# Kernel optimization log

Hardware: AMD Instinct MI355X
Metric: run time of the kernel (lower is better)

The kernel has to match this reference:

```python
import jax, jax.numpy as jnp
import numpy as np

N, D_FEAT, P, E, L, H, D = 20000, 256, 3, 60000, 4, 8, 32  # d = H*D = 256


def _l2norm(x, axis):
    return x / jnp.maximum(jnp.linalg.norm(x, axis=axis, keepdims=True), 1e-12)


def _gru_last_hidden(edata, w_ih, w_hh, b_ih, b_hh):
    # edata: [E, L, d]; torch nn.GRU gate math, return final hidden [E, d]
    d = w_hh.shape[1]
    def step(h, x):
        gi = x @ w_ih.T + b_ih          # [E, 3d]
        gh = h @ w_hh.T + b_hh
        i_r, i_z, i_n = jnp.split(gi, 3, axis=-1)
        h_r, h_z, h_n = jnp.split(gh, 3, axis=-1)
        r = jax.nn.sigmoid(i_r + h_r)
        z = jax.nn.sigmoid(i_z + h_z)
        n = jnp.tanh(i_n + r * h_n)
        return (1.0 - z) * n + z * h, None
    h0 = jnp.zeros((edata.shape[0], d), edata.dtype)
    h, _ = jax.lax.scan(step, h0, jnp.swapaxes(edata, 0, 1))
    return h


def setup_inputs() -> dict:
    key = jax.random.key(0)
    ks = jax.random.split(key, 10)
    d = H * D
    s = 1.0 / np.sqrt(d)
    return {
        "features": jax.random.normal(ks[0], (N, D_FEAT), jnp.float32),
        "gru_w_ih": jax.random.uniform(ks[1], (P, 3 * d, d), jnp.float32, -s, s),
        "gru_w_hh": jax.random.uniform(ks[2], (P, 3 * d, d), jnp.float32, -s, s),
        "gru_b_ih": jax.random.uniform(ks[3], (P, 3 * d), jnp.float32, -s, s),
        "gru_b_hh": jax.random.uniform(ks[4], (P, 3 * d), jnp.float32, -s, s),
        "fc1_w": jax.random.normal(ks[5], (D, D), jnp.float32) * (1.414 / np.sqrt(D)),
        "fc2": jax.random.normal(ks[6], (H, D), jnp.float32) * (1.414 / np.sqrt(D)),
        "edge_metapath_indices": jax.random.randint(ks[7], (P, E, L), 0, N),
        "edge_dst": jax.random.randint(ks[8], (P, E), 0, N),
    }


def reference(features, gru_w_ih, gru_w_hh, gru_b_ih, gru_b_hh, fc1_w, fc2,
              edge_metapath_indices, edge_dst):
    # node features, normalized across heads (F.normalize default dim=1)
    ft = _l2norm(features.reshape(N, H, D), axis=1)          # [N, H, D]
    metapath_outs = []
    for p in range(P):  # small fixed loop over structurally distinct metapaths
        edata = features[edge_metapath_indices[p]]           # [E, L, d] gather
        hidden = _gru_last_hidden(edata, gru_w_ih[p], gru_w_hh[p],
                                  gru_b_ih[p], gru_b_hh[p])  # [E, d]
        eft = _l2norm(hidden.reshape(E, H, D), axis=1)       # [E, H, D]
        dst = edge_dst[p]                                    # [E]
        sim = jnp.sum(eft * ft[dst], axis=-1)                # [E, H]
        a = jax.nn.softmax(sim, axis=-1)[..., None]          # softmax over heads (faithful)
        nft = jax.ops.segment_sum(eft * a, dst, num_segments=N)  # [N, H, D]
        metapath_outs.append(nft)
    h = jnp.stack(metapath_outs, axis=0)                     # [P, N, H, D]
    # semantic attention across metapaths: fc1 (no bias) then fc2 scoring
    s = jnp.mean(jnp.sum(jnp.tanh(jnp.einsum('pnhd,ed->pnhe', h, fc1_w)) * fc2,
                         axis=(2, 3)), axis=1)               # [P]
    beta = jax.nn.softmax(s)
    out = jnp.einsum('p,pnhd->nhd', beta, h).reshape(N, H * D)
    return out
```

## Files before the change

### kernel.cpp

```cpp
#include <hip/hip_runtime.h>
#include <math.h>


typedef unsigned short u16;
typedef unsigned int u32;
typedef __bf16 bf16x8 __attribute__((ext_vector_type(8)));
typedef short short8 __attribute__((ext_vector_type(8)));
typedef float f32x4 __attribute__((ext_vector_type(4)));

#define N_NODES 20000
#define P_META 3
#define E_EDGES 60000
#define L_STEPS 4
#define DMODEL 256
#define G3 768
#define M_TILE 32
#define TILES_PER_P 1875
#define G_TILES 313

__device__ __forceinline__ float bf2f(u16 b) {
  u32 u = ((u32)b) << 16; float f; __builtin_memcpy(&f, &u, 4); return f;
}
__device__ __forceinline__ u16 f2bf(float f) {
  u32 u; __builtin_memcpy(&u, &f, 4);
  return (u16)((u + 0x7FFFu + ((u >> 16) & 1u)) >> 16);
}
__device__ __forceinline__ u16 f2h(float f) {
  _Float16 h = (_Float16)f; u16 u; __builtin_memcpy(&u, &h, 2); return u;
}
__device__ __forceinline__ float h2f(u16 u) {
  _Float16 h; __builtin_memcpy(&h, &u, 2); return (float)h;
}
__device__ __forceinline__ short8 load8(const void* base, int isbf, size_t off) {
  if (isbf) return *(const short8*)((const u16*)base + off);
  const float* f = (const float*)base + off;
  const float4 a = *(const float4*)f;
  const float4 b = *(const float4*)(f + 4);
  short8 r;
  r[0] = (short)f2bf(a.x); r[1] = (short)f2bf(a.y);
  r[2] = (short)f2bf(a.z); r[3] = (short)f2bf(a.w);
  r[4] = (short)f2bf(b.x); r[5] = (short)f2bf(b.y);
  r[6] = (short)f2bf(b.z); r[7] = (short)f2bf(b.w);
  return r;
}
__device__ __forceinline__ float loadS(const void* base, int isbf, size_t off) {
  return isbf ? bf2f(((const u16*)base)[off]) : ((const float*)base)[off];
}
static __device__ __forceinline__ f32x4 mfma16(short8 a, short8 b, f32x4 c) {
  return __builtin_amdgcn_mfma_f32_16x16x32_bf16(
      __builtin_bit_cast(bf16x8, a), __builtin_bit_cast(bf16x8, b), c, 0, 0, 0);
}
__device__ __forceinline__ float sigm(float x) { return 1.0f / (1.0f + __expf(-x)); }
__device__ __forceinline__ float ftanh(float x) { return 1.0f - 2.0f / (__expf(2.0f * x) + 1.0f); }

__global__ void sniff_kernel(const void* __restrict__ feat, int* __restrict__ flag) {
  const int i = threadIdx.x;
  const u16 e = ((const u16*)feat)[2 * i];
  const int ex = (e >> 7) & 0xFF;
  const bool sane = (e == 0) || (ex >= 103 && ex <= 143);
  const unsigned long long b = __ballot(sane);
  if (i == 0) *flag = (__popcll(b) >= 32) ? 1 : 0;
}

__global__ void pack_weights_kernel(const void* __restrict__ w_ih,
                                    const void* __restrict__ w_hh,
                                    u16* __restrict__ Wpk,
                                    const int* __restrict__ dflag) {
  const int isbf = *dflag;
  const int g = blockIdx.x * 256 + threadIdx.x;
  const int fb = g >> 6, ln = g & 63;
  const int k0 = fb & 7, c = (fb >> 3) & 15, pm = fb >> 7;
  const int p = pm / 6, mat = pm - p * 6;
  const int gate = (mat >= 3) ? mat - 3 : mat;
  const void* W = (mat >= 3) ? w_hh : w_ih;
  const size_t src = ((size_t)p * G3 + gate * 256 + c * 16 + (ln & 15)) * DMODEL
                     + k0 * 32 + (ln >> 4) * 8;
  short8 v = load8(W, isbf, src);
  *(short8*)(Wpk + (size_t)fb * 512 + ln * 8) = v;
}

__global__ void pack_feat_kernel(const void* __restrict__ features,
                                 u16* __restrict__ Fpk,
                                 float* __restrict__ invf,
                                 const int* __restrict__ dflag) {
  const int isbf = *dflag;
  const int n = blockIdx.x * 8 + (threadIdx.x >> 5);
  const int dd = threadIdx.x & 31;
  float v[8]; float ss = 0.f;
  #pragma unroll
  for (int hh = 0; hh < 8; ++hh) {
    v[hh] = loadS(features, isbf, (size_t)n * DMODEL + hh * 32 + dd);
    ss += v[hh] * v[hh];
  }
  invf[(size_t)n * 32 + dd] = 1.0f / fmaxf(sqrtf(ss), 1e-12f);
  #pragma unroll
  for (int hh = 0; hh < 8; ++hh)
    Fpk[(size_t)n * DMODEL + hh * 32 + dd] = f2bf(v[hh]);
}

__global__ void pack_bias_kernel(const void* __restrict__ b_ih,
                                 const void* __restrict__ b_hh,
                                 float* __restrict__ bpk,
                                 const int* __restrict__ dflag) {
  const int isbf = *dflag;
  const int g = blockIdx.x * 256 + threadIdx.x;
  const int p = g / 1536, r = g - p * 1536;
  const int gi = r >> 8, j = r & 255;
  const float v = (gi < 3) ? loadS(b_ih, isbf, (size_t)p * G3 + gi * 256 + j)
                           : loadS(b_hh, isbf, (size_t)p * G3 + (gi - 3) * 256 + j);
  bpk[g] = v;
}

__global__ __launch_bounds__(256, 4) void gih_kernel(
    const u16* __restrict__ Fpk, const u16* __restrict__ Wpk,
    const float* __restrict__ bpk, u16* __restrict__ Gpk,
    u16* __restrict__ H1pk, int p0, int multi)
{
  __shared__ u16 Xb[64 * 256];
  __shared__ float Bs[1536];
  const int tid = threadIdx.x;
  const int bx = blockIdx.x;
  int pb = 0, tile = bx;
  if (multi) { pb = bx / G_TILES; tile = bx - pb * G_TILES; }
  const int p = p0 + pb;
  u16* Gp  = Gpk  + (size_t)pb * (size_t)N_NODES * 1024;
  u16* H1p = H1pk + (size_t)pb * (size_t)N_NODES * DMODEL;
  const int r0 = tile * 64;
  const int wv = tid >> 6, ln = tid & 63;
  const int n16 = ln & 15, quad = ln >> 4;
  const int cbase = wv * 4;

  for (int i = tid; i < 1536; i += 256) Bs[i] = bpk[(size_t)p * 1536 + i];

  const int m4 = tid >> 2, seg = tid & 3, swm = m4 & 7;
  {
    int rr = r0 + m4; if (rr >= N_NODES) rr = N_NODES - 1;
    const u16* frp = Fpk + (size_t)rr * DMODEL;
    #pragma unroll
    for (int u = 0; u < 8; ++u) {
      short8 xv = *(const short8*)(frp + (seg * 8 + u) * 8);
      *(short8*)(Xb + m4 * 256 + (((seg * 8 + u) ^ swm) << 3)) = xv;
    }
  }
  __syncthreads();

  #pragma unroll 1
  for (int ci = 0; ci < 4; ++ci) {
    const int c = cbase + ci;
    const f32x4 z4 = {0.f, 0.f, 0.f, 0.f};
    f32x4 aR[4], aZ[4], aN[4];
    #pragma unroll
    for (int rt = 0; rt < 4; ++rt) { aR[rt] = z4; aZ[rt] = z4; aN[rt] = z4; }
    const u16* wb0 = Wpk + ((size_t)(p * 6 * 16 + c) * 8) * 512 + ln * 8;
    #pragma unroll 2
    for (int k0 = 0; k0 < 8; ++k0) {
      const int un = (((k0 * 4 + quad) ^ (n16 & 7)) << 3);
      const u16* xr = Xb + n16 * 256 + un;
      short8 x0 = *(const short8*)(xr);
      short8 x1 = *(const short8*)(xr + 4096);
      short8 x2 = *(const short8*)(xr + 8192);
      short8 x3 = *(const short8*)(xr + 12288);
      const u16* wk = wb0 + k0 * 512;
      short8 b0 = *(const short8*)(wk);
      short8 b1 = *(const short8*)(wk + 65536);
      short8 b2 = *(const short8*)(wk + 131072);
      aR[0] = mfma16(x0, b0, aR[0]); aR[1] = mfma16(x1, b0, aR[1]);
      aR[2] = mfma16(x2, b0, aR[2]); aR[3] = mfma16(x3, b0, aR[3]);
      aZ[0] = mfma16(x0, b1, aZ[0]); aZ[1] = mfma16(x1, b1, aZ[1]);
      aZ[2] = mfma16(x2, b1, aZ[2]); aZ[3] = mfma16(x3, b1, aZ[3]);
      aN[0] = mfma16(x0, b2, aN[0]); aN[1] = mfma16(x1, b2, aN[1]);
      aN[2] = mfma16(x2, b2, aN[2]); aN[3] = mfma16(x3, b2, aN[3]);
    }
    const int j = c * 16 + n16;
    const float br  = Bs[j],        bz  = Bs[256 + j],  bn  = Bs[512 + j];
    const float bhr = Bs[768 + j],  bhz = Bs[1024 + j], bhn = Bs[1280 + j];
    #pragma unroll
    for (int rt = 0; rt < 4; ++rt) {
      #pragma unroll
      for (int i = 0; i < 4; ++i) {
        const int row = r0 + rt * 16 + quad * 4 + i;
        if (row < N_NODES) {
          const float grb = aR[rt][i] + br + bhr;
          const float gzb = aZ[rt][i] + bz + bhz;
          const float gn  = aN[rt][i] + bn;
          const float rr = sigm(grb);
          const float zz = sigm(gzb);
          const float nn = ftanh(gn + rr * bhn);
          const u16 h1 = f2bf((1.0f - zz) * nn);
          uint2 st;
          st.x = (u32)f2h(grb) | ((u32)f2h(gzb) << 16);
          st.y = (u32)f2h(gn) | ((u32)h1 << 16);
          *(uint2*)(Gp + (size_t)row * 1024 + j * 4) = st;
          H1p[(size_t)row * DMODEL + j] = h1;
        }
      }
    }
  }
}

__global__ __launch_bounds__(256, 4) void gru2_edge_kernel(
    const u16*  __restrict__ Fpk,
    const u16*  __restrict__ Wpk,
    const u16*  __restrict__ Gpk,
    const u16*  __restrict__ H1pk,
    const float* __restrict__ bpk,
    const float* __restrict__ invf,
    const int*  __restrict__ emi,
    const int*  __restrict__ edst,
    float*      __restrict__ nft,
    int p0, int multi)
{
  __shared__ u16 HH[2][32 * 256];
  __shared__ float Bsh[256];
  __shared__ int emiS[128];
  __shared__ u16 invhs16[32 * 32];
  __shared__ u16 aws16[32 * 8];

  const int tid  = threadIdx.x;
  const int bx   = blockIdx.x;
  int pb = 0, tile = bx;
  if (multi) { pb = bx / TILES_PER_P; tile = bx - pb * TILES_PER_P; }
  const int p = p0 + pb;
  const u16* Gp  = Gpk  + (size_t)pb * (size_t)N_NODES * 1024;
  const u16* H1p = H1pk + (size_t)pb * (size_t)N_NODES * DMODEL;
  const int e0   = tile * M_TILE;
  const int wv   = tid >> 6;
  const int ln   = tid & 63;
  const int n16  = ln & 15;
  const int quad = ln >> 4;
  const int cbase = wv * 4;

  Bsh[tid & 255] = bpk[(size_t)p * 1536 + 1280 + (tid & 255)];
  if (tid < 128) {
    const int el = tid >> 2, l = tid & 3;
    emiS[tid] = emi[((size_t)p * E_EDGES + e0 + el) * L_STEPS + l];
  }

  {
    const int m8 = tid >> 3, seg = tid & 7, swm = m8 & 7;
    const int f0 = emi[((size_t)p * E_EDGES + e0 + m8) * L_STEPS];
    const u16* hp = H1p + (size_t)f0 * DMODEL;
    #pragma unroll
    for (int t = 0; t < 4; ++t) {
      const int u = seg * 4 + t;
      short8 xv = *(const short8*)(hp + u * 8);
      *(short8*)(&HH[0][m8 * 256 + ((u ^ swm) << 3)]) = xv;
    }
  }

  uint2 gi[8];

  #pragma unroll 1
  for (int step = 1; step < L_STEPS; ++step) {
    __syncthreads();
    const u16* Ard = &HH[(step & 1) ^ 1][0];
    u16*       Bwr = &HH[step & 1][0];

    if (step == 1) {
      #pragma unroll
      for (int rt = 0; rt < 2; ++rt) {
        #pragma unroll
        for (int i = 0; i < 4; ++i) {
          const int mm = rt * 16 + quad * 4 + i;
          const u32 off = (u32)emiS[mm * 4 + 1] * 2048u + (u32)(n16 * 8)
                          + (u32)(cbase * 128);
          gi[rt * 4 + i] = *(const uint2*)((const char*)Gp + off);
        }
      }
    }

    #pragma unroll 1
    for (int ci = 0; ci < 4; ++ci) {
      const int c = cbase + ci;
      const f32x4 z4 = {0.f, 0.f, 0.f, 0.f};
      f32x4 aHR[2], aHZ[2], aHN[2];
      #pragma unroll
      for (int rt = 0; rt < 2; ++rt) { aHR[rt] = z4; aHZ[rt] = z4; aHN[rt] = z4; }
      const u16* wb0 = Wpk + ((size_t)((p * 6 + 3) * 16 + c) * 8) * 512 + ln * 8;
      #pragma unroll 2
      for (int k0 = 0; k0 < 8; ++k0) {
        const int un = (((k0 * 4 + quad) ^ (n16 & 7)) << 3);
        const u16* hr = Ard + n16 * 256 + un;
        short8 hv0 = *(const short8*)(hr);
        short8 hv1 = *(const short8*)(hr + 4096);
        const u16* wk = wb0 + k0 * 512;
        short8 b3 = *(const short8*)(wk);
        short8 b4 = *(const short8*)(wk + 65536);
        short8 b5 = *(const short8*)(wk + 131072);
        aHR[0] = mfma16(hv0, b3, aHR[0]); aHR[1] = mfma16(hv1, b3, aHR[1]);
        aHZ[0] = mfma16(hv0, b4, aHZ[0]); aHZ[1] = mfma16(hv1, b4, aHZ[1]);
        aHN[0] = mfma16(hv0, b5, aHN[0]); aHN[1] = mfma16(hv1, b5, aHN[1]);
      }
      const int j = c * 16 + n16;
      const float bhn = Bsh[j];
      const int ju = ((j >> 3) << 3), jl = j & 7;
      const int dopref = (ci < 3) || (step < 3);
      const int nstep = (ci < 3) ? step : step + 1;
      const int nc    = (ci < 3) ? c + 1 : cbase;
      #pragma unroll
      for (int rt = 0; rt < 2; ++rt) {
        #pragma unroll
        for (int i = 0; i < 4; ++i) {
          const int v = rt * 4 + i;
          const int mm = rt * 16 + quad * 4 + i;
          const uint2 g = gi[v];
          if (dopref) {
            const u32 off = (u32)emiS[mm * 4 + nstep] * 2048u + (u32)(n16 * 8)
                            + (u32)(nc * 128);
            gi[v] = *(const uint2*)((const char*)Gp + off);
          }
          const float grb = h2f((u16)(g.x & 0xFFFFu));
          const float gzb = h2f((u16)(g.x >> 16));
          const float gn  = h2f((u16)(g.y & 0xFFFFu));
          const float r  = sigm(grb + aHR[rt][i]);
          const float z  = sigm(gzb + aHZ[rt][i]);
          const float ng = ftanh(gn + r * (aHN[rt][i] + bhn));
          const int hoff = mm * 256 + (ju ^ ((mm & 7) << 3)) + jl;
          const float hold = bf2f(Ard[hoff]);
          Bwr[hoff] = f2bf((1.0f - z) * ng + z * hold);
        }
      }
    }
  }
  __syncthreads();
  const u16* Hf = &HH[1][0];

  const int m = tid >> 3, q = tid & 7;
  const int dstn = edst[(size_t)p * E_EDGES + e0 + m];

  ushort4 hq[8], fq[8];
  #pragma unroll
  for (int hh = 0; hh < 8; ++hh) {
    const int unit = 4 * hh + (q >> 1);
    hq[hh] = *(const ushort4*)(Hf + m * 256 + ((unit ^ (m & 7)) << 3) + (q & 1) * 4);
    fq[hh] = *(const ushort4*)(Fpk + (size_t)dstn * DMODEL + hh * 32 + q * 4);
  }
  const float4 ivf4 = *(const float4*)(invf + (size_t)dstn * 32 + q * 4);
  const float invfv[4] = {ivf4.x, ivf4.y, ivf4.z, ivf4.w};

  float invh[4];
  #pragma unroll
  for (int t = 0; t < 4; ++t) {
    float sh = 0.f;
    #pragma unroll
    for (int hh = 0; hh < 8; ++hh) {
      const float hv = bf2f((&hq[hh].x)[t]);
      sh += hv * hv;
    }
    invh[t] = 1.0f / fmaxf(sqrtf(sh), 1e-12f);
  }
  float sim[8];
  #pragma unroll
  for (int hh = 0; hh < 8; ++hh) {
    float s = 0.f;
    #pragma unroll
    for (int t = 0; t < 4; ++t)
      s += (bf2f((&hq[hh].x)[t]) * invh[t]) * (bf2f((&fq[hh].x)[t]) * invfv[t]);
    sim[hh] = s;
  }
  #pragma unroll
  for (int hh = 0; hh < 8; ++hh) {
    sim[hh] += __shfl_xor(sim[hh], 1, 64);
    sim[hh] += __shfl_xor(sim[hh], 2, 64);
    sim[hh] += __shfl_xor(sim[hh], 4, 64);
  }
  float mx = sim[0];
  #pragma unroll
  for (int hh = 1; hh < 8; ++hh) mx = fmaxf(mx, sim[hh]);
  float aw[8], se = 0.f;
  #pragma unroll
  for (int hh = 0; hh < 8; ++hh) { aw[hh] = __expf(sim[hh] - mx); se += aw[hh]; }
  const float sinv = 1.0f / se;

  #pragma unroll
  for (int t = 0; t < 4; ++t) invhs16[m * 32 + q * 4 + t] = f2h(invh[t]);
  if (q == 0) {
    #pragma unroll
    for (int hh = 0; hh < 8; ++hh) aws16[m * 8 + hh] = f2h(aw[hh] * sinv);
  }
  __syncthreads();

  const int esub = ln >> 4;
  const int li   = ln & 15;
  #pragma unroll
  for (int pp = 0; pp < 2; ++pp) {
    const int em = wv * 8 + pp * 4 + esub;
    const int dn = edst[(size_t)p * E_EDGES + e0 + em];
    float* op = nft + ((size_t)p * N_NODES + dn) * DMODEL;
    const u16* ivh = invhs16 + em * 32;
    const u16* awp = aws16 + em * 8;
    #pragma unroll
    for (int t = 0; t < 16; ++t) {
      const int idx = t * 16 + li;
      const u16 hb = Hf[em * 256 + ((((idx >> 3) ^ (em & 7))) << 3) + (idx & 7)];
      const float val = bf2f(hb) * h2f(ivh[idx & 31]) * h2f(awp[idx >> 5]);
      atomicAdd(op + idx, val);
    }
  }
}

__global__ void semantic_score_kernel(const float* __restrict__ nft,
                                      const void* __restrict__ fc1,
                                      const void* __restrict__ fc2,
                                      float* __restrict__ s_out,
                                      const int* __restrict__ dflag) {
  __shared__ float fc1s[32 * 32];
  __shared__ float fc2s[8 * 32];
  __shared__ float red[4];
  const int isbf = *dflag;
  const int tid = threadIdx.x;
  for (int i = tid; i < 1024; i += 256) fc1s[i] = loadS(fc1, isbf, i);
  for (int i = tid; i < 256; i += 256) fc2s[i] = loadS(fc2, isbf, i);
  __syncthreads();
  const int p = blockIdx.y;
  const int g = blockIdx.x * 256 + tid;
  const int n = g >> 3, hh = g & 7;
  const float* hrow = nft + ((size_t)p * N_NODES + n) * DMODEL + hh * 32;
  float hv[32];
  #pragma unroll
  for (int d4 = 0; d4 < 8; ++d4) {
    const float4 v = *(const float4*)(hrow + d4 * 4);
    hv[d4 * 4 + 0] = v.x; hv[d4 * 4 + 1] = v.y; hv[d4 * 4 + 2] = v.z; hv[d4 * 4 + 3] = v.w;
  }
  float acc = 0.f;
  for (int e = 0; e < 32; ++e) {
    float t = 0.f;
    #pragma unroll
    for (int d = 0; d < 32; ++d) t += hv[d] * fc1s[e * 32 + d];
    acc += ftanh(t) * fc2s[hh * 32 + e];
  }
  #pragma unroll
  for (int o = 32; o > 0; o >>= 1) acc += __shfl_xor(acc, o, 64);
  if ((tid & 63) == 0) red[tid >> 6] = acc;
  __syncthreads();
  if (tid == 0) atomicAdd(&s_out[p], red[0] + red[1] + red[2] + red[3]);
}

__global__ void combine_kernel(const float* __restrict__ nft,
                               const float* __restrict__ s_in,
                               void* __restrict__ out,
                               const int* __restrict__ dflag) {
  const int isbf = *dflag;
  const float inv_n = 1.0f / (float)N_NODES;
  const float s0 = s_in[0] * inv_n, s1 = s_in[1] * inv_n, s2 = s_in[2] * inv_n;
  const float mx = fmaxf(s0, fmaxf(s1, s2));
  const float x0 = __expf(s0 - mx), x1 = __expf(s1 - mx), x2 = __expf(s2 - mx);
  const float inv = 1.0f / (x0 + x1 + x2);
  const float w0 = x0 * inv, w1 = x1 * inv, w2 = x2 * inv;
  const size_t stride = (size_t)N_NODES * DMODEL;
  const size_t idx = ((size_t)blockIdx.x * 256 + threadIdx.x) * 4;
  if (idx >= stride) return;
  const float4 a = *(const float4*)(nft + idx);
  const float4 b = *(const float4*)(nft + stride + idx);
  const float4 c = *(const float4*)(nft + 2 * stride + idx);
  const float o0 = w0 * a.x + w1 * b.x + w2 * c.x;
  const float o1 = w0 * a.y + w1 * b.y + w2 * c.y;
  const float o2 = w0 * a.z + w1 * b.z + w2 * c.z;
  const float o3 = w0 * a.w + w1 * b.w + w2 * c.w;
  if (isbf) {
    ushort4 r; r.x = f2bf(o0); r.y = f2bf(o1); r.z = f2bf(o2); r.w = f2bf(o3);
    *(ushort4*)((u16*)out + idx) = r;
  } else {
    float4 r; r.x = o0; r.y = o1; r.z = o2; r.w = o3;
    *(float4*)((float*)out + idx) = r;
  }
}

__global__ void fill_diag_kernel(u16* __restrict__ out, int n) {
  int i = (blockIdx.x * 256 + threadIdx.x) * 8;
  if (i + 8 <= n) {
    const int v = 0x3E003E00;
    int4 w; w.x = v; w.y = v; w.z = v; w.w = v;
    *(int4*)(out + i) = w;
  } else {
    for (; i < n; ++i) out[i] = 0x3E00;
  }
}

extern "C" void kernel_launch(void* const* d_in, const int* in_sizes, int n_in,
                              void* d_out, int out_size, void* d_ws, size_t ws_size,
                              hipStream_t stream) {
  const void* features = d_in[0];
  const void* w_ih     = d_in[1];
  const void* w_hh     = d_in[2];
  const void* b_ih     = d_in[3];
  const void* b_hh     = d_in[4];
  const void* fc1      = d_in[5];
  const void* fc2      = d_in[6];
  const int*  emi      = (const int*)d_in[7];
  const int*  edst     = (const int*)d_in[8];

  const size_t NFT_F   = (size_t)P_META * N_NODES * DMODEL;
  const size_t OFF_WPK = NFT_F + 8;
  const size_t OFF_FPK = OFF_WPK + 589824;
  const size_t OFF_INV = OFF_FPK + 2560000;
  const size_t OFF_BPK = OFF_INV + 640000;
  const size_t OFF_GPK = OFF_BPK + 4608;
  const size_t GPK_PF  = (size_t)N_NODES * 1024 / 2;
  const size_t H1_PF   = (size_t)N_NODES * DMODEL / 2;
  const size_t OFF_H1_FULL = OFF_GPK + 3 * GPK_PF;
  const size_t NEED_FULL   = (OFF_H1_FULL + 3 * H1_PF) * sizeof(float);
  const size_t OFF_H1_LOOP = OFF_GPK + GPK_PF;
  const size_t NEED_LOOP   = (OFF_H1_LOOP + H1_PF) * sizeof(float);

  if (ws_size < NEED_LOOP) {
    fill_diag_kernel<<<dim3((out_size / 8 + 255) / 256), 256, 0, stream>>>((u16*)d_out, out_size);
    return;
  }
  const int full = (ws_size >= NEED_FULL) ? 1 : 0;

  float* wsf  = (float*)d_ws;
  float* nft  = wsf;
  float* s_ws = wsf + NFT_F;
  int*   flag = (int*)(wsf + NFT_F + 3);
  u16*   Wpk  = (u16*)(wsf + OFF_WPK);
  u16*   Fpk  = (u16*)(wsf + OFF_FPK);
  float* invf = wsf + OFF_INV;
  float* bpk  = wsf + OFF_BPK;
  u16*   Gpk  = (u16*)(wsf + OFF_GPK);
  u16*   H1pk = (u16*)(wsf + (full ? OFF_H1_FULL : OFF_H1_LOOP));

  hipMemsetAsync(d_ws, 0, (NFT_F + 8) * sizeof(float), stream);
  sniff_kernel<<<1, 64, 0, stream>>>(features, flag);
  pack_weights_kernel<<<dim3(576), 256, 0, stream>>>(w_ih, w_hh, Wpk, flag);
  pack_feat_kernel<<<dim3(2500), 256, 0, stream>>>(features, Fpk, invf, flag);
  pack_bias_kernel<<<dim3(18), 256, 0, stream>>>(b_ih, b_hh, bpk, flag);
  if (full) {
    gih_kernel<<<dim3(P_META * G_TILES), 256, 0, stream>>>(Fpk, Wpk, bpk, Gpk, H1pk, 0, 1);
    gru2_edge_kernel<<<dim3(P_META * TILES_PER_P), 256, 0, stream>>>(
        Fpk, Wpk, Gpk, H1pk, bpk, invf, emi, edst, nft, 0, 1);
  } else {
    for (int p = 0; p < P_META; ++p) {
      gih_kernel<<<dim3(G_TILES), 256, 0, stream>>>(Fpk, Wpk, bpk, Gpk, H1pk, p, 0);
      gru2_edge_kernel<<<dim3(TILES_PER_P), 256, 0, stream>>>(
          Fpk, Wpk, Gpk, H1pk, bpk, invf, emi, edst, nft, p, 0);
    }
  }
  semantic_score_kernel<<<dim3(625, 3), 256, 0, stream>>>(nft, fc1, fc2, s_ws, flag);
  combine_kernel<<<dim3(5000), 256, 0, stream>>>(nft, s_ws, d_out, flag);
}
```

Measured before the change: 734.5 us.

## Double gru2_edge_kernel block to 512 threads, splitting gate columns across 8 waves

Raises the recurrent GRU/edge kernel from 4 to 8 waves per block. Each wave now handles 2 column chunks instead of 4, and the epilogue uses 16 lanes per edge with an extra shuffle stage. The goal is more parallelism per tile and more latency hiding for the gathered gate loads. In exchange, the launch bound asks for 8 blocks of 512 threads per CU, which may force register spilling or limit real occupancy. The weight B-fragment loads are also now duplicated across more waves.

```diff
diff --git a/kernel.cpp b/kernel.cpp
--- a/kernel.cpp
+++ b/kernel.cpp
@@ -198,7 +198,7 @@
   }
 }
 
-__global__ __launch_bounds__(256, 4) void gru2_edge_kernel(
+__global__ __launch_bounds__(512, 8) void gru2_edge_kernel(
     const u16*  __restrict__ Fpk,
     const u16*  __restrict__ Wpk,
     const u16*  __restrict__ Gpk,
@@ -228,23 +228,24 @@
   const int ln   = tid & 63;
   const int n16  = ln & 15;
   const int quad = ln >> 4;
-  const int cbase = wv * 4;
-
-  Bsh[tid & 255] = bpk[(size_t)p * 1536 + 1280 + (tid & 255)];
-  if (tid < 128) {
-    const int el = tid >> 2, l = tid & 3;
-    emiS[tid] = emi[((size_t)p * E_EDGES + e0 + el) * L_STEPS + l];
+  const int cbase = wv * 2;
+
+  if (tid < 256) Bsh[tid] = bpk[(size_t)p * 1536 + 1280 + tid];
+  if (tid >= 256 && tid < 384) {
+    const int t = tid - 256;
+    const int el = t >> 2, l = t & 3;
+    emiS[t] = emi[((size_t)p * E_EDGES + e0 + el) * L_STEPS + l];
   }
 
   {
-    const int m8 = tid >> 3, seg = tid & 7, swm = m8 & 7;
-    const int f0 = emi[((size_t)p * E_EDGES + e0 + m8) * L_STEPS];
+    const int m16 = tid >> 4, seg = tid & 15, swm = m16 & 7;
+    const int f0 = emi[((size_t)p * E_EDGES + e0 + m16) * L_STEPS];
     const u16* hp = H1p + (size_t)f0 * DMODEL;
     #pragma unroll
-    for (int t = 0; t < 4; ++t) {
-      const int u = seg * 4 + t;
+    for (int t = 0; t < 2; ++t) {
+      const int u = seg * 2 + t;
       short8 xv = *(const short8*)(hp + u * 8);
-      *(short8*)(&HH[0][m8 * 256 + ((u ^ swm) << 3)]) = xv;
+      *(short8*)(&HH[0][m16 * 256 + ((u ^ swm) << 3)]) = xv;
     }
   }
 
@@ -270,7 +271,7 @@
     }
 
     #pragma unroll 1
-    for (int ci = 0; ci < 4; ++ci) {
+    for (int ci = 0; ci < 2; ++ci) {
       const int c = cbase + ci;
       const f32x4 z4 = {0.f, 0.f, 0.f, 0.f};
       f32x4 aHR[2], aHZ[2], aHN[2];
@@ -294,9 +295,9 @@
       const int j = c * 16 + n16;
       const float bhn = Bsh[j];
       const int ju = ((j >> 3) << 3), jl = j & 7;
-      const int dopref = (ci < 3) || (step < 3);
-      const int nstep = (ci < 3) ? step : step + 1;
-      const int nc    = (ci < 3) ? c + 1 : cbase;
+      const int dopref = (ci < 1) || (step < 3);
+      const int nstep = (ci < 1) ? step : step + 1;
+      const int nc    = (ci < 1) ? c + 1 : cbase;
       #pragma unroll
       for (int rt = 0; rt < 2; ++rt) {
         #pragma unroll
@@ -325,22 +326,22 @@
   __syncthreads();
   const u16* Hf = &HH[1][0];
 
-  const int m = tid >> 3, q = tid & 7;
+  const int m = tid >> 4, q = tid & 15;
   const int dstn = edst[(size_t)p * E_EDGES + e0 + m];
 
-  ushort4 hq[8], fq[8];
+  ushort2 hq[8], fq[8];
   #pragma unroll
   for (int hh = 0; hh < 8; ++hh) {
-    const int unit = 4 * hh + (q >> 1);
-    hq[hh] = *(const ushort4*)(Hf + m * 256 + ((unit ^ (m & 7)) << 3) + (q & 1) * 4);
-    fq[hh] = *(const ushort4*)(Fpk + (size_t)dstn * DMODEL + hh * 32 + q * 4);
-  }
-  const float4 ivf4 = *(const float4*)(invf + (size_t)dstn * 32 + q * 4);
-  const float invfv[4] = {ivf4.x, ivf4.y, ivf4.z, ivf4.w};
-
-  float invh[4];
-  #pragma unroll
-  for (int t = 0; t < 4; ++t) {
+    const int unit = 4 * hh + (q >> 2);
+    hq[hh] = *(const ushort2*)(Hf + m * 256 + ((unit ^ (m & 7)) << 3) + (q & 3) * 2);
+    fq[hh] = *(const ushort2*)(Fpk + (size_t)dstn * DMODEL + hh * 32 + q * 2);
+  }
+  const float2 ivf2 = *(const float2*)(invf + (size_t)dstn * 32 + q * 2);
+  const float invfv[2] = {ivf2.x, ivf2.y};
+
+  float invh[2];
+  #pragma unroll
+  for (int t = 0; t < 2; ++t) {
     float sh = 0.f;
     #pragma unroll
     for (int hh = 0; hh < 8; ++hh) {
@@ -354,7 +355,7 @@
   for (int hh = 0; hh < 8; ++hh) {
     float s = 0.f;
     #pragma unroll
-    for (int t = 0; t < 4; ++t)
+    for (int t = 0; t < 2; ++t)
       s += (bf2f((&hq[hh].x)[t]) * invh[t]) * (bf2f((&fq[hh].x)[t]) * invfv[t]);
     sim[hh] = s;
   }
@@ -363,6 +364,7 @@
     sim[hh] += __shfl_xor(sim[hh], 1, 64);
     sim[hh] += __shfl_xor(sim[hh], 2, 64);
     sim[hh] += __shfl_xor(sim[hh], 4, 64);
+    sim[hh] += __shfl_xor(sim[hh], 8, 64);
   }
   float mx = sim[0];
   #pragma unroll
@@ -373,7 +375,7 @@
   const float sinv = 1.0f / se;
 
   #pragma unroll
-  for (int t = 0; t < 4; ++t) invhs16[m * 32 + q * 4 + t] = f2h(invh[t]);
+  for (int t = 0; t < 2; ++t) invhs16[m * 32 + q * 2 + t] = f2h(invh[t]);
   if (q == 0) {
     #pragma unroll
     for (int hh = 0; hh < 8; ++hh) aws16[m * 8 + hh] = f2h(aw[hh] * sinv);
@@ -382,9 +384,8 @@
 
   const int esub = ln >> 4;
   const int li   = ln & 15;
-  #pragma unroll
-  for (int pp = 0; pp < 2; ++pp) {
-    const int em = wv * 8 + pp * 4 + esub;
+  {
+    const int em = wv * 4 + esub;
     const int dn = edst[(size_t)p * E_EDGES + e0 + em];
     float* op = nft + ((size_t)p * N_NODES + dn) * DMODEL;
     const u16* ivh = invhs16 + em * 32;
@@ -527,12 +528,12 @@
   pack_bias_kernel<<<dim3(18), 256, 0, stream>>>(b_ih, b_hh, bpk, flag);
   if (full) {
     gih_kernel<<<dim3(P_META * G_TILES), 256, 0, stream>>>(Fpk, Wpk, bpk, Gpk, H1pk, 0, 1);
-    gru2_edge_kernel<<<dim3(P_META * TILES_PER_P), 256, 0, stream>>>(
+    gru2_edge_kernel<<<dim3(P_META * TILES_PER_P), 512, 0, stream>>>(
         Fpk, Wpk, Gpk, H1pk, bpk, invf, emi, edst, nft, 0, 1);
   } else {
     for (int p = 0; p < P_META; ++p) {
       gih_kernel<<<dim3(G_TILES), 256, 0, stream>>>(Fpk, Wpk, bpk, Gpk, H1pk, p, 0);
-      gru2_edge_kernel<<<dim3(TILES_PER_P), 256, 0, stream>>>(
+      gru2_edge_kernel<<<dim3(TILES_PER_P), 512, 0, stream>>>(
           Fpk, Wpk, Gpk, H1pk, bpk, invf, emi, edst, nft, p, 0);
     }
   }
```

New measurement: 1.158 ms. 1.58x slower.
